# Kernel optimization log

Hardware: AMD Instinct MI355X
Metric: run time of the kernel (lower is better)

The kernel has to match this reference:

```python
import jax, jax.numpy as jnp
import numpy as np

N_NODES = 50000
N_EDGES = 800000
FEAT_DIM = 64


def setup_inputs() -> dict:
    key = jax.random.key(0)
    k1, k2, k3 = jax.random.split(key, 3)
    x = jax.random.normal(k1, (N_NODES, FEAT_DIM), dtype=jnp.float32)
    beta = jnp.ones((1,), dtype=jnp.float32)
    # CSR-equivalent edge list: sorted destination rows + random source columns
    row_index = jnp.sort(jax.random.randint(k2, (N_EDGES,), 0, N_NODES, dtype=jnp.int32))
    col_index = jax.random.randint(k3, (N_EDGES,), 0, N_NODES, dtype=jnp.int32)
    return {"x": x, "beta": beta, "row_index": row_index, "col_index": col_index}


def reference(x, beta, row_index, col_index):
    """AGNN layer: SDDMM edge attention (beta * cosine similarity) over the
    sparse graph, per-row softmax, then sparse neighbor aggregation.
    Equivalent math to mygraph.SDDMM + mygraph.agnn_udf (select_id == 5).
    x: [N, D]; row_index/col_index: [E] edge endpoints (row = destination).
    """
    N = x.shape[0]
    eps = 1e-8
    # L2-normalize node features for cosine similarity
    xn = x * jax.lax.rsqrt(jnp.sum(x * x, axis=-1, keepdims=True) + eps)  # [N, D]
    # SDDMM: attention only on existing edges
    att = beta[0] * jnp.sum(xn[row_index] * xn[col_index], axis=-1)  # [E]
    # Numerically stable segment softmax over each destination row
    m = jax.ops.segment_max(att, row_index, num_segments=N)  # [N]
    m = jnp.where(jnp.isfinite(m), m, 0.0)  # empty rows -> -inf guard
    e = jnp.exp(att - m[row_index])  # [E]
    denom = jax.ops.segment_sum(e, row_index, num_segments=N)  # [N]
    alpha = e / jnp.maximum(denom[row_index], 1e-16)  # [E]
    # Sparse aggregation: out_i = sum_j alpha_ij * x_j
    out = jax.ops.segment_sum(alpha[:, None] * x[col_index], row_index, num_segments=N)
    return out
```

## Files before the change

kernel.cpp:

```cpp
#include <hip/hip_runtime.h>
#include <hip/hip_fp16.h>

#define FEAT 64

typedef _Float16 h2 __attribute__((ext_vector_type(2)));
union HU { uint u; h2 h; };
__device__ inline h2   u2h(uint u) { HU x; x.u = u; return x.h; }
__device__ inline uint h2u(h2 h)   { HU x; x.h = h; return x.u; }
__device__ inline uint packh2f(float lo, float hi) {
    h2 v; v[0] = (_Float16)lo; v[1] = (_Float16)hi; return h2u(v);
}

__device__ inline float dot8(uint4 q, h2 x0, h2 x1, h2 x2, h2 x3) {
#if __has_builtin(__builtin_amdgcn_fdot2)
    float d = __builtin_amdgcn_fdot2(u2h(q.x), x0, 0.f, false);
    d = __builtin_amdgcn_fdot2(u2h(q.y), x1, d, false);
    d = __builtin_amdgcn_fdot2(u2h(q.z), x2, d, false);
    d = __builtin_amdgcn_fdot2(u2h(q.w), x3, d, false);
    return d;
#else
    h2 a = u2h(q.x), b = u2h(q.y), c = u2h(q.z), e = u2h(q.w);
    return (float)a[0]*(float)x0[0] + (float)a[1]*(float)x0[1]
         + (float)b[0]*(float)x1[0] + (float)b[1]*(float)x1[1]
         + (float)c[0]*(float)x2[0] + (float)c[1]*(float)x2[1]
         + (float)e[0]*(float)x3[0] + (float)e[1]*(float)x3[1];
#endif
}

__global__ void prep1_kernel(const float* __restrict__ x,
                             float* __restrict__ rn,
                             float* __restrict__ nrm,
                             uint4* __restrict__ xhn,
                             const int* __restrict__ row,
                             int* __restrict__ row_ptr,
                             int N, int E, int normBlocks) {
    if ((int)blockIdx.x < normBlocks) {
        int wid  = blockIdx.x * (blockDim.x >> 6) + (threadIdx.x >> 6);
        int lane = threadIdx.x & 63;
        int g    = lane >> 3;
        int sub  = lane & 7;
        int r    = wid * 8 + g;
        if (r >= N) return;
        const char* xB = (const char*)x;
        uint roff = ((uint)r << 8) + ((uint)sub << 4);
        float4 xa = *reinterpret_cast<const float4*>(xB + roff);
        float4 xb = *reinterpret_cast<const float4*>(xB + roff + 128);
        float q = xa.x*xa.x + xa.y*xa.y + xa.z*xa.z + xa.w*xa.w
                + xb.x*xb.x + xb.y*xb.y + xb.z*xb.z + xb.w*xb.w;
        q += __shfl_xor(q, 1);
        q += __shfl_xor(q, 2);
        q += __shfl_xor(q, 4);
        float qe  = q + 1e-8f;
        float rnr = rsqrtf(qe);
        if (sub == 0) { rn[r] = rnr; nrm[r] = qe * rnr; }
        uint4 p;
        p.x = packh2f(xa.x * rnr, xa.y * rnr);
        p.y = packh2f(xa.z * rnr, xa.w * rnr);
        p.z = packh2f(xb.x * rnr, xb.y * rnr);
        p.w = packh2f(xb.z * rnr, xb.w * rnr);
        xhn[r * 8 + sub] = p;
    } else {
        int e = (blockIdx.x - normBlocks) * blockDim.x + threadIdx.x;
        if (e >= E) return;
        int curr = row[e];
        if (e == 0) {
            for (int r = 0; r <= curr; ++r) row_ptr[r] = 0;
        } else {
            int prev = row[e - 1];
            for (int r = prev + 1; r <= curr; ++r) row_ptr[r] = e;
        }
        if (e == E - 1) {
            for (int r = curr + 1; r <= N; ++r) row_ptr[r] = E;
        }
    }
}

__global__ void prep2_kernel(const int* __restrict__ col,
                             const float* __restrict__ nrm,
                             int2* __restrict__ zip, int E) {
    int e = blockIdx.x * blockDim.x + threadIdx.x;
    if (e >= E) return;
    int c = col[e];
    zip[e] = make_int2(c, __float_as_int(nrm[c]));
}

__global__ void fused_kernel(const float* __restrict__ x,
                             const uint4* __restrict__ xhn,
                             const float* __restrict__ rn,
                             const float* __restrict__ beta,
                             const int* __restrict__ row_ptr,
                             const int2* __restrict__ zip,
                             float* __restrict__ out, int N) {
    int wid  = blockIdx.x * (blockDim.x >> 6) + (threadIdx.x >> 6);
    int lane = threadIdx.x & 63;
    int g    = lane >> 3;
    int sub  = lane & 7;
    int r    = wid * 8 + g;
    bool rv  = (r < N);

    int start = 0, deg = 0;
    if (rv) {
        start = row_ptr[r];
        deg   = row_ptr[r + 1] - start;
    }

    h2 xr0, xr1, xr2, xr3;
    {
        float4 xa = make_float4(0.f, 0.f, 0.f, 0.f);
        float4 xb = make_float4(0.f, 0.f, 0.f, 0.f);
        if (rv) {
            const char* xB = (const char*)x;
            uint roff = ((uint)r << 8) + ((uint)sub << 4);
            xa = *reinterpret_cast<const float4*>(xB + roff);
            xb = *reinterpret_cast<const float4*>(xB + roff + 128);
            float brn = beta[0] * rn[r];
            xa.x *= brn; xa.y *= brn; xa.z *= brn; xa.w *= brn;
            xb.x *= brn; xb.y *= brn; xb.z *= brn; xb.w *= brn;
        }
        xr0 = u2h(packh2f(xa.x, xa.y));
        xr1 = u2h(packh2f(xa.z, xa.w));
        xr2 = u2h(packh2f(xb.x, xb.y));
        xr3 = u2h(packh2f(xb.z, xb.w));
    }

    int2 zipA = make_int2(0, 0), zipB = make_int2(0, 0);
    if (sub < deg)     zipA = zip[start + sub];
    if (8 + sub < deg) zipB = zip[start + 8 + sub];

    int   c0 = __shfl(zipA.x, 0, 8), c1 = __shfl(zipA.x, 1, 8);
    int   c2 = __shfl(zipA.x, 2, 8), c3 = __shfl(zipA.x, 3, 8);
    float n0 = __shfl(__int_as_float(zipA.y), 0, 8);
    float n1 = __shfl(__int_as_float(zipA.y), 1, 8);
    float n2 = __shfl(__int_as_float(zipA.y), 2, 8);
    float n3 = __shfl(__int_as_float(zipA.y), 3, 8);
    uint4 q0 = xhn[(uint)c0 * 8u + sub], q1 = xhn[(uint)c1 * 8u + sub];
    uint4 q2 = xhn[(uint)c2 * 8u + sub], q3 = xhn[(uint)c3 * 8u + sub];

    float  s  = 0.f;
    float4 aa = make_float4(0.f, 0.f, 0.f, 0.f);
    float4 ab = make_float4(0.f, 0.f, 0.f, 0.f);

    for (int base = 0; base < deg; base += 4) {
        if (base && (base & 7) == 0) {
            zipA = zipB;
            zipB = make_int2(0, 0);
            if (base + 8 + sub < deg) zipB = zip[start + base + 8 + sub];
        }
        int  nkk = (base + 4) & 7;
        int2 cS  = (nkk == 4) ? zipA : zipB;
        int   nc0 = __shfl(cS.x, nkk + 0, 8), nc1 = __shfl(cS.x, nkk + 1, 8);
        int   nc2 = __shfl(cS.x, nkk + 2, 8), nc3 = __shfl(cS.x, nkk + 3, 8);
        float nn0 = __shfl(__int_as_float(cS.y), nkk + 0, 8);
        float nn1 = __shfl(__int_as_float(cS.y), nkk + 1, 8);
        float nn2 = __shfl(__int_as_float(cS.y), nkk + 2, 8);
        float nn3 = __shfl(__int_as_float(cS.y), nkk + 3, 8);
        uint4 nq0 = xhn[(uint)nc0 * 8u + sub], nq1 = xhn[(uint)nc1 * 8u + sub];
        uint4 nq2 = xhn[(uint)nc2 * 8u + sub], nq3 = xhn[(uint)nc3 * 8u + sub];

        float d0 = dot8(q0, xr0, xr1, xr2, xr3);
        float d1 = dot8(q1, xr0, xr1, xr2, xr3);
        float d2 = dot8(q2, xr0, xr1, xr2, xr3);
        float d3 = dot8(q3, xr0, xr1, xr2, xr3);
        d0 += __shfl_xor(d0, 1);  d1 += __shfl_xor(d1, 1);
        d2 += __shfl_xor(d2, 1);  d3 += __shfl_xor(d3, 1);
        d0 += __shfl_xor(d0, 2);  d1 += __shfl_xor(d1, 2);
        d2 += __shfl_xor(d2, 2);  d3 += __shfl_xor(d3, 2);
        d0 += __shfl_xor(d0, 4);  d1 += __shfl_xor(d1, 4);
        d2 += __shfl_xor(d2, 4);  d3 += __shfl_xor(d3, 4);

        float e0 = (base + 0 < deg) ? __expf(d0) : 0.f;
        float e1 = (base + 1 < deg) ? __expf(d1) : 0.f;
        float e2 = (base + 2 < deg) ? __expf(d2) : 0.f;
        float e3 = (base + 3 < deg) ? __expf(d3) : 0.f;
        s += (e0 + e1) + (e2 + e3);

        float w0 = e0 * n0, w1 = e1 * n1, w2 = e2 * n2, w3 = e3 * n3;
        h2 wh0; wh0[0] = (_Float16)w0; wh0[1] = wh0[0];
        h2 wh1; wh1[0] = (_Float16)w1; wh1[1] = wh1[0];
        h2 wh2; wh2[0] = (_Float16)w2; wh2[1] = wh2[0];
        h2 wh3; wh3[0] = (_Float16)w3; wh3[1] = wh3[0];

        h2 p0 = u2h(q0.x) * wh0;  p0 = u2h(q1.x) * wh1 + p0;
        p0 = u2h(q2.x) * wh2 + p0;  p0 = u2h(q3.x) * wh3 + p0;
        h2 p1 = u2h(q0.y) * wh0;  p1 = u2h(q1.y) * wh1 + p1;
        p1 = u2h(q2.y) * wh2 + p1;  p1 = u2h(q3.y) * wh3 + p1;
        h2 p2 = u2h(q0.z) * wh0;  p2 = u2h(q1.z) * wh1 + p2;
        p2 = u2h(q2.z) * wh2 + p2;  p2 = u2h(q3.z) * wh3 + p2;
        h2 p3 = u2h(q0.w) * wh0;  p3 = u2h(q1.w) * wh1 + p3;
        p3 = u2h(q2.w) * wh2 + p3;  p3 = u2h(q3.w) * wh3 + p3;

        aa.x += (float)p0[0];  aa.y += (float)p0[1];
        aa.z += (float)p1[0];  aa.w += (float)p1[1];
        ab.x += (float)p2[0];  ab.y += (float)p2[1];
        ab.z += (float)p3[0];  ab.w += (float)p3[1];

        q0 = nq0; q1 = nq1; q2 = nq2; q3 = nq3;
        n0 = nn0; n1 = nn1; n2 = nn2; n3 = nn3;
    }

    float inv = 1.0f / fmaxf(s, 1e-16f);
    if (rv) {
        uint roff = ((uint)r << 8) + ((uint)sub << 4);
        *reinterpret_cast<float4*>((char*)out + roff) =
            make_float4(aa.x * inv, aa.y * inv, aa.z * inv, aa.w * inv);
        *reinterpret_cast<float4*>((char*)out + roff + 128) =
            make_float4(ab.x * inv, ab.y * inv, ab.z * inv, ab.w * inv);
    }
}

extern "C" void kernel_launch(void* const* d_in, const int* in_sizes, int n_in,
                              void* d_out, int out_size, void* d_ws, size_t ws_size,
                              hipStream_t stream) {
    const float* x    = (const float*)d_in[0];
    const float* beta = (const float*)d_in[1];
    const int*   row  = (const int*)d_in[2];
    const int*   col  = (const int*)d_in[3];
    float*       out  = (float*)d_out;

    const int N = in_sizes[0] / FEAT;
    const int E = in_sizes[2];

    char*  ws = (char*)d_ws;
    size_t o  = 0;
    auto alloc = [&](size_t bytes) {
        size_t cur = o;
        o = (o + bytes + 511) & ~(size_t)511;
        return cur;
    };
    float* rn      = (float*)(ws + alloc((size_t)N * 4));
    float* nrm     = (float*)(ws + alloc((size_t)N * 4));
    int*   row_ptr = (int*)  (ws + alloc((size_t)(N + 1) * 4));
    int2*  zip     = (int2*) (ws + alloc((size_t)E * 8));
    uint4* xhn     = (uint4*)(ws + alloc((size_t)N * 128));

    {
        int normBlocks = (N + 31) / 32;
        int edgeBlocks = (E + 255) / 256;
        prep1_kernel<<<normBlocks + edgeBlocks, 256, 0, stream>>>(
            x, rn, nrm, xhn, row, row_ptr, N, E, normBlocks);
    }
    {
        int grid = (E + 255) / 256;
        prep2_kernel<<<grid, 256, 0, stream>>>(col, nrm, zip, E);
    }
    {
        int waves = (N + 7) / 8;
        int grid  = (waves + 3) / 4;
        fused_kernel<<<grid, 256, 0, stream>>>(
            x, xhn, rn, beta, row_ptr, zip, out, N);
    }
}
```

Measured before the change: 38.53 us.

## Prefetch neighbor feature rows into an LDS ring via async global_load_lds

Replaces the register-based one-step prefetch of gathered half-precision neighbor rows with a per-wave 8-slot LDS ring. The ring is filled by global_load_lds direct-to-LDS loads issued two steps ahead, throttled with explicit s_waitcnt vmcnt/lgkmcnt. The aim is to keep more gather loads in flight and hide the latency of the random neighbor accesses while freeing prefetch registers. In exchange it adds LDS traffic and reads, relies on hand-placed wait counts that depend on the order the compiler issues loads, and hardcodes four waves per block.

```diff
diff --git a/kernel.cpp b/kernel.cpp
--- a/kernel.cpp
+++ b/kernel.cpp
@@ -26,6 +26,11 @@
          + (float)e[0]*(float)x3[0] + (float)e[1]*(float)x3[1];
 #endif
 }
+
+#define GL_LDS(SRC, DST)                                                     \
+    __builtin_amdgcn_global_load_lds(                                        \
+        (const __attribute__((address_space(1))) void*)(SRC),                \
+        (__attribute__((address_space(3))) void*)(DST), 16, 0, 0)
 
 __global__ void prep1_kernel(const float* __restrict__ x,
                              float* __restrict__ rn,
@@ -91,10 +96,12 @@
                              const int* __restrict__ row_ptr,
                              const int2* __restrict__ zip,
                              float* __restrict__ out, int N) {
-    int wid  = blockIdx.x * (blockDim.x >> 6) + (threadIdx.x >> 6);
+    __shared__ uint4 ring[4][8][64];
+    int wv   = threadIdx.x >> 6;
     int lane = threadIdx.x & 63;
     int g    = lane >> 3;
     int sub  = lane & 7;
+    int wid  = blockIdx.x * 4 + wv;
     int r    = wid * 8 + g;
     bool rv  = (r < N);
 
@@ -127,35 +134,46 @@
     if (sub < deg)     zipA = zip[start + sub];
     if (8 + sub < deg) zipB = zip[start + 8 + sub];
 
-    int   c0 = __shfl(zipA.x, 0, 8), c1 = __shfl(zipA.x, 1, 8);
-    int   c2 = __shfl(zipA.x, 2, 8), c3 = __shfl(zipA.x, 3, 8);
-    float n0 = __shfl(__int_as_float(zipA.y), 0, 8);
-    float n1 = __shfl(__int_as_float(zipA.y), 1, 8);
-    float n2 = __shfl(__int_as_float(zipA.y), 2, 8);
-    float n3 = __shfl(__int_as_float(zipA.y), 3, 8);
-    uint4 q0 = xhn[(uint)c0 * 8u + sub], q1 = xhn[(uint)c1 * 8u + sub];
-    uint4 q2 = xhn[(uint)c2 * 8u + sub], q3 = xhn[(uint)c3 * 8u + sub];
+    #pragma unroll
+    for (int j = 0; j < 8; ++j) {
+        int cj = __shfl(zipA.x, j, 8);
+        GL_LDS(xhn + (uint)cj * 8u + sub, &ring[wv][j][0]);
+    }
 
     float  s  = 0.f;
     float4 aa = make_float4(0.f, 0.f, 0.f, 0.f);
     float4 ab = make_float4(0.f, 0.f, 0.f, 0.f);
 
     for (int base = 0; base < deg; base += 4) {
-        if (base && (base & 7) == 0) {
+        asm volatile("s_waitcnt vmcnt(4)" ::: "memory");
+        int s0 = base & 7;
+        uint4 q0 = ring[wv][s0 + 0][lane];
+        uint4 q1 = ring[wv][s0 + 1][lane];
+        uint4 q2 = ring[wv][s0 + 2][lane];
+        uint4 q3 = ring[wv][s0 + 3][lane];
+        asm volatile("s_waitcnt lgkmcnt(0)" ::: "memory");
+
+        if (base && s0 == 0) {
             zipA = zipB;
             zipB = make_int2(0, 0);
             if (base + 8 + sub < deg) zipB = zip[start + base + 8 + sub];
         }
-        int  nkk = (base + 4) & 7;
-        int2 cS  = (nkk == 4) ? zipA : zipB;
-        int   nc0 = __shfl(cS.x, nkk + 0, 8), nc1 = __shfl(cS.x, nkk + 1, 8);
-        int   nc2 = __shfl(cS.x, nkk + 2, 8), nc3 = __shfl(cS.x, nkk + 3, 8);
-        float nn0 = __shfl(__int_as_float(cS.y), nkk + 0, 8);
-        float nn1 = __shfl(__int_as_float(cS.y), nkk + 1, 8);
-        float nn2 = __shfl(__int_as_float(cS.y), nkk + 2, 8);
-        float nn3 = __shfl(__int_as_float(cS.y), nkk + 3, 8);
-        uint4 nq0 = xhn[(uint)nc0 * 8u + sub], nq1 = xhn[(uint)nc1 * 8u + sub];
-        uint4 nq2 = xhn[(uint)nc2 * 8u + sub], nq3 = xhn[(uint)nc3 * 8u + sub];
+
+        float n0 = __shfl(__int_as_float(zipA.y), s0 + 0, 8);
+        float n1 = __shfl(__int_as_float(zipA.y), s0 + 1, 8);
+        float n2 = __shfl(__int_as_float(zipA.y), s0 + 2, 8);
+        float n3 = __shfl(__int_as_float(zipA.y), s0 + 3, 8);
+
+        {
+            int c0n = __shfl(zipB.x, s0 + 0, 8);
+            int c1n = __shfl(zipB.x, s0 + 1, 8);
+            int c2n = __shfl(zipB.x, s0 + 2, 8);
+            int c3n = __shfl(zipB.x, s0 + 3, 8);
+            GL_LDS(xhn + (uint)c0n * 8u + sub, &ring[wv][s0 + 0][0]);
+            GL_LDS(xhn + (uint)c1n * 8u + sub, &ring[wv][s0 + 1][0]);
+            GL_LDS(xhn + (uint)c2n * 8u + sub, &ring[wv][s0 + 2][0]);
+            GL_LDS(xhn + (uint)c3n * 8u + sub, &ring[wv][s0 + 3][0]);
+        }
 
         float d0 = dot8(q0, xr0, xr1, xr2, xr3);
         float d1 = dot8(q1, xr0, xr1, xr2, xr3);
@@ -193,10 +211,9 @@
         aa.z += (float)p1[0];  aa.w += (float)p1[1];
         ab.x += (float)p2[0];  ab.y += (float)p2[1];
         ab.z += (float)p3[0];  ab.w += (float)p3[1];
-
-        q0 = nq0; q1 = nq1; q2 = nq2; q3 = nq3;
-        n0 = nn0; n1 = nn1; n2 = nn2; n3 = nn3;
-    }
+    }
+
+    asm volatile("s_waitcnt vmcnt(0)" ::: "memory");
 
     float inv = 1.0f / fmaxf(s, 1e-16f);
     if (rv) {
```

Result: slower. 44.66 us (+15.9%).
